# Optimization experiments

Measured on AMD Instinct MI355X. Metric: run time of the kernel, lower is better.

Reference implementation:

```python
import jax, jax.numpy as jnp
import numpy as np

N, B, D = 2048, 2, 512
H, R = 8, 3
C = D // H  # head dim = 64


def setup_inputs() -> dict:
    key = jax.random.key(0)
    ks = jax.random.split(key, 12)
    x_q = jax.random.normal(ks[0], (N, B, D), jnp.float32)
    x_k = jax.random.normal(ks[1], (N, B, D), jnp.float32)
    x_v = jax.random.normal(ks[2], (N, B, D), jnp.float32)
    attn_mask = jax.random.randint(ks[3], (B, R, N, N), 0, 2).astype(bool)
    # pad the last 128 key positions (realistic padding; avoids all -inf rows)
    key_padding_mask = jnp.zeros((B, N), bool).at[:, -128:].set(True)
    s = 1.0 / np.sqrt(D)
    Wq = jax.random.normal(ks[4], (D, D), jnp.float32) * s
    Wk = jax.random.normal(ks[5], (D, D), jnp.float32) * s
    Wv = jax.random.normal(ks[6], (D, D), jnp.float32) * s
    Wo = jax.random.normal(ks[7], (D, D), jnp.float32) * s
    bq = jnp.zeros((D,), jnp.float32)
    bk = jnp.zeros((D,), jnp.float32)
    bv = jnp.zeros((D,), jnp.float32)
    bo = jnp.zeros((D,), jnp.float32)
    # mask_weight: randn, last column set to sqrt(head_dim) as in __init__
    mask_weight = jax.random.normal(ks[8], (H, R + 1), jnp.float32)
    mask_weight = mask_weight.at[:, -1].set(np.sqrt(C))
    return dict(x_q=x_q, x_k=x_k, x_v=x_v, attn_mask=attn_mask,
                key_padding_mask=key_padding_mask, Wq=Wq, bq=bq, Wk=Wk, bk=bk,
                Wv=Wv, bv=bv, Wo=Wo, bo=bo, mask_weight=mask_weight)


def _split_heads(x):
    # (n, b, h*c) -> (b, h, n, c)
    n, b, _ = x.shape
    return jnp.transpose(x.reshape(n, b, H, C), (1, 2, 0, 3))


def reference(x_q, x_k, x_v, attn_mask, key_padding_mask,
              Wq, bq, Wk, bk, Wv, bv, Wo, bo, mask_weight):
    q = _split_heads(x_q @ Wq + bq)  # (b,h,n,c)
    k = _split_heads(x_k @ Wk + bk)
    v = _split_heads(x_v @ Wv + bv)

    # relative bias: softmax over edge-type weights, scaled per head
    rel_w = jax.nn.softmax(mask_weight[:, :-1], axis=-1)  # (h,r)
    inv_mask = (~attn_mask).astype(jnp.float32)           # (b,r,n,m)
    rel = jnp.einsum('hr,h,brnm->bhnm', rel_w, mask_weight[:, -1], inv_mask)
    rel = jnp.where(key_padding_mask[:, None, None, :], -jnp.inf, rel)

    # scaled dot-product attention (torch default scale = 1/sqrt(head_dim))
    scores = jnp.einsum('bhnc,bhmc->bhnm', q, k) * (1.0 / np.sqrt(C))
    attn = jax.nn.softmax(scores + rel, axis=-1)
    o = jnp.einsum('bhnm,bhmc->bhnc', attn, v)

    # (b,h,n,c) -> (n,b,h*c)
    n = o.shape[2]
    o = jnp.transpose(o, (2, 0, 1, 3)).reshape(n, o.shape[0], H * C)
    return o @ Wo + bo
```

## Files before the change

kernel.cpp:

```cpp
#include <hip/hip_runtime.h>
#include <hip/hip_bf16.h>

#define NN 2048
#define LOG2E 1.4426950408889634f

typedef unsigned int u32;
typedef unsigned short u16;
typedef unsigned char u8;

typedef __attribute__((ext_vector_type(8))) short short8;
typedef __attribute__((ext_vector_type(4))) float f32x4;

__device__ __forceinline__ u16 f2bf(float f){
  __hip_bfloat16 h = __float2bfloat16(f);
  return *reinterpret_cast<u16*>(&h);
}
__device__ __forceinline__ float bf1(u16 u){ return __uint_as_float(((u32)u) << 16); }
__device__ __forceinline__ u32 pack2(float a, float b){
  return (u32)f2bf(a) | ((u32)f2bf(b) << 16);
}
__device__ __forceinline__ void gload16(const void* g, void* l){
  __builtin_amdgcn_global_load_lds((const __attribute__((address_space(1))) u32*)g,
                                   (__attribute__((address_space(3))) u32*)l, 16, 0, 0);
}

__global__ __launch_bounds__(256)
void prep_k(const int* __restrict__ am, const int* __restrict__ kp,
            u8* __restrict__ cmb)
{
  const size_t tid  = (size_t)blockIdx.x * 256 + threadIdx.x;
  const size_t base = tid * 4;
  const int row = (int)(base >> 11);
  const int m0  = (int)(base & 2047);
  const int b = row >> 11, n = row & 2047;
  const size_t e0 = (((size_t)(b*3) * NN) + n) * NN + m0;
  const int4 a0 = *reinterpret_cast<const int4*>(am + e0);
  const int4 a1 = *reinterpret_cast<const int4*>(am + e0 + (size_t)NN*NN);
  const int4 a2 = *reinterpret_cast<const int4*>(am + e0 + 2*(size_t)NN*NN);
  const int4 kv = *reinterpret_cast<const int4*>(kp + (size_t)b*NN + m0);
  const int a0v[4] = {a0.x,a0.y,a0.z,a0.w};
  const int a1v[4] = {a1.x,a1.y,a1.z,a1.w};
  const int a2v[4] = {a2.x,a2.y,a2.z,a2.w};
  const int kvv[4] = {kv.x,kv.y,kv.z,kv.w};
  uchar4 out;
  u8* o = (u8*)&out;
  #pragma unroll
  for (int i = 0; i < 4; ++i)
    o[i] = (u8)((a0v[i]?1:0) | (a1v[i]?2:0) | (a2v[i]?4:0) | (kvv[i]?8:0));
  *reinterpret_cast<uchar4*>(cmb + base) = out;
}

__global__ __launch_bounds__(256)
void trw4_k(const float* __restrict__ W0, const float* __restrict__ W1,
            const float* __restrict__ W2, const float* __restrict__ W3,
            u16* __restrict__ WT)
{
  __shared__ float tile[32][33];
  const int zz = blockIdx.z;
  const float* W = (zz == 0) ? W0 : (zz == 1) ? W1 : (zz == 2) ? W2 : W3;
  u16* dst = WT + (size_t)zz * 262144;
  const int t = threadIdx.x;
  const int k0 = blockIdx.x * 32, n0 = blockIdx.y * 32;
  const int c = t & 31, r = t >> 5;
  #pragma unroll
  for (int i = 0; i < 4; ++i)
    tile[r + 8*i][c] = W[(size_t)(k0 + r + 8*i) * 512 + n0 + c];
  __syncthreads();
  #pragma unroll
  for (int i = 0; i < 4; ++i)
    dst[(size_t)(n0 + r + 8*i) * 512 + k0 + c] = f2bf(tile[c][r + 8*i]);
}

__global__ __launch_bounds__(256)
void trw_k(const float* __restrict__ W, u16* __restrict__ WT)
{
  __shared__ float tile[32][33];
  const int t = threadIdx.x;
  const int k0 = blockIdx.x * 32, n0 = blockIdx.y * 32;
  const int c = t & 31, r = t >> 5;
  #pragma unroll
  for (int i = 0; i < 4; ++i)
    tile[r + 8*i][c] = W[(size_t)(k0 + r + 8*i) * 512 + n0 + c];
  __syncthreads();
  #pragma unroll
  for (int i = 0; i < 4; ++i)
    WT[(size_t)(n0 + r + 8*i) * 512 + k0 + c] = f2bf(tile[c][r + 8*i]);
}

template<int BN, bool SCATTER, bool ABF16, bool OUTF32>
__device__ __forceinline__
void gemm_core(const void* __restrict__ Av, const u16* __restrict__ WT,
               const float* __restrict__ bias, void* __restrict__ Cd,
               float scale, int m0, int n0)
{
  constexpr int NI  = BN / 64;
  constexpr int WNL = BN / 32;
  __shared__ u16 As[2][64*64];
  __shared__ u16 Ws[2][BN*64];

  const int t = threadIdx.x;
  const int lane = t & 63;
  const int w = t >> 6;
  const int g = lane >> 4, r15 = lane & 15;
  const int wn = w * (BN/4);

  const int arow = t >> 2, akc = (t & 3) * 16, as0 = (t & 3) * 2;
  const int wrn = (BN==128) ? (t>>1) : (t>>2);
  const int wkc = (BN==128) ? ((t&1)*32) : ((t&3)*16);
  const int wsb = (BN==128) ? ((t&1)*4)  : ((t&3)*2);

  uint4  war[WNL];
  uint4  aab[2];
  float4 aaf[4];

  auto loadA = [&](int k0){
    if constexpr (ABF16) {
      const u16* A = (const u16*)Av;
      aab[0] = *reinterpret_cast<const uint4*>(A + (size_t)(m0+arow)*512 + k0 + akc);
      aab[1] = *reinterpret_cast<const uint4*>(A + (size_t)(m0+arow)*512 + k0 + akc + 8);
    } else {
      const float* A = (const float*)Av;
      #pragma unroll
      for (int q = 0; q < 4; ++q)
        aaf[q] = *reinterpret_cast<const float4*>(A + (size_t)(m0+arow)*512 + k0 + akc + 4*q);
    }
  };
  auto loadW = [&](int k0){
    #pragma unroll
    for (int i = 0; i < WNL; ++i)
      war[i] = *reinterpret_cast<const uint4*>(WT + (size_t)(n0+wrn)*512 + k0 + wkc + 8*i);
  };
  auto writeA = [&](int bf){
    uint4 v0, v1;
    if constexpr (ABF16) { v0 = aab[0]; v1 = aab[1]; }
    else {
      v0.x = pack2(aaf[0].x, aaf[0].y); v0.y = pack2(aaf[0].z, aaf[0].w);
      v0.z = pack2(aaf[1].x, aaf[1].y); v0.w = pack2(aaf[1].z, aaf[1].w);
      v1.x = pack2(aaf[2].x, aaf[2].y); v1.y = pack2(aaf[2].z, aaf[2].w);
      v1.z = pack2(aaf[3].x, aaf[3].y); v1.w = pack2(aaf[3].z, aaf[3].w);
    }
    *reinterpret_cast<uint4*>(&As[bf][arow*64 + (((as0  ) ^ (arow&7)) << 3)]) = v0;
    *reinterpret_cast<uint4*>(&As[bf][arow*64 + (((as0+1) ^ (arow&7)) << 3)]) = v1;
  };
  auto writeW = [&](int bf){
    #pragma unroll
    for (int i = 0; i < WNL; ++i)
      *reinterpret_cast<uint4*>(&Ws[bf][wrn*64 + (((wsb+i) ^ (wrn&7)) << 3)]) = war[i];
  };

  const f32x4 fz = {0.f,0.f,0.f,0.f};
  f32x4 acc[4][NI];
  #pragma unroll
  for (int mi = 0; mi < 4; ++mi)
    #pragma unroll
    for (int ni = 0; ni < NI; ++ni) acc[mi][ni] = fz;

  loadA(0); loadW(0);
  writeA(0); writeW(0);
  __syncthreads();

  for (int kt = 0; kt < 8; ++kt) {
    const int cur = kt & 1;
    if (kt < 7) { loadA((kt+1)*64); loadW((kt+1)*64); }
    #pragma unroll
    for (int ks = 0; ks < 2; ++ks) {
      short8 bfr[NI], afr[4];
      #pragma unroll
      for (int ni = 0; ni < NI; ++ni) {
        const int n = wn + 16*ni + r15;
        bfr[ni] = *reinterpret_cast<const short8*>(&Ws[cur][n*64 + (((ks*4+g) ^ (n&7)) << 3)]);
      }
      #pragma unroll
      for (int mi = 0; mi < 4; ++mi) {
        const int m = 16*mi + r15;
        afr[mi] = *reinterpret_cast<const short8*>(&As[cur][m*64 + (((ks*4+g) ^ (m&7)) << 3)]);
      }
      #pragma unroll
      for (int mi = 0; mi < 4; ++mi)
        #pragma unroll
        for (int ni = 0; ni < NI; ++ni)
          acc[mi][ni] = __builtin_amdgcn_mfma_f32_16x16x32_bf16(afr[mi], bfr[ni], acc[mi][ni], 0, 0, 0);
    }
    if (kt < 7) { writeA(cur^1); writeW(cur^1); }
    __syncthreads();
  }

  float bia[NI];
  #pragma unroll
  for (int ni = 0; ni < NI; ++ni) bia[ni] = bias[n0 + wn + 16*ni + r15];
  #pragma unroll
  for (int mi = 0; mi < 4; ++mi) {
    #pragma unroll
    for (int ni = 0; ni < NI; ++ni) {
      #pragma unroll
      for (int j = 0; j < 4; ++j) {
        const int row = m0 + 16*mi + 4*g + j;
        const int col = n0 + wn + 16*ni + r15;
        const float v = (acc[mi][ni][j] + bia[ni]) * scale;
        if constexpr (SCATTER) {
          const int bb = row & 1, ntok = row >> 1;
          const int h = col >> 6, c = col & 63;
          ((u16*)Cd)[(((size_t)(bb*8 + h) * NN + ntok) * 64) + c] = f2bf(v);
        } else if constexpr (OUTF32) {
          ((float*)Cd)[(size_t)row * 512 + col] = v;
        } else {
          ((u16*)Cd)[(size_t)row * 512 + col] = f2bf(v);
        }
      }
    }
  }
}

__global__ __launch_bounds__(256)
void gemm_qkv(const float* __restrict__ x0, const float* __restrict__ x1,
              const float* __restrict__ x2, const u16* __restrict__ WT3,
              const float* __restrict__ b0, const float* __restrict__ b1,
              const float* __restrict__ b2, u16* __restrict__ dst, float qscale)
{
  const int z = blockIdx.z;
  const float* A    = (z == 0) ? x0 : (z == 1) ? x1 : x2;
  const float* bias = (z == 0) ? b0 : (z == 1) ? b1 : b2;
  gemm_core<128, true, false, false>(A, WT3 + (size_t)z*262144, bias,
                                     dst + (size_t)z*2097152,
                                     (z == 0) ? qscale : 1.0f,
                                     blockIdx.x*64, blockIdx.y*128);
}

__global__ __launch_bounds__(256)
void gemm_wo(const u16* __restrict__ Ob, const u16* __restrict__ WT,
             const float* __restrict__ bias, float* __restrict__ out)
{
  gemm_core<64, false, true, true>(Ob, WT, bias, out, 1.0f,
                                   blockIdx.x*64, blockIdx.y*64);
}

__global__ __launch_bounds__(512)
void attn_mfma(const u16* __restrict__ Q, const u16* __restrict__ K,
               const u16* __restrict__ V, const u8* __restrict__ cmb,
               const float* __restrict__ mw, u16* __restrict__ O,
               u16* __restrict__ Opart, float2* __restrict__ Ml, int kspan)
{
  __shared__ u16 Ks[2][64*64];
  __shared__ u16 Vs[2][64*64];
  __shared__ u16 Ps[8][16*64];
  __shared__ float lut[16];

  const int t = threadIdx.x;
  const int lane = t & 63;
  const int w = t >> 6;
  const int g = lane >> 4;
  const int r15 = lane & 15;
  const int bh = blockIdx.y;
  const int z = blockIdx.z;
  const int b = bh >> 3, h = bh & 7;
  const int n0 = blockIdx.x * 128;
  const int nq = n0 + w*16 + r15;
  const int k_beg = z * kspan;
  const float NEGINF = -__builtin_inff();

  if (t < 16) {
    const float mw0 = mw[h*4+0], mw1 = mw[h*4+1], mw2 = mw[h*4+2];
    const float msc = mw[h*4+3];
    const float mxw = fmaxf(mw0, fmaxf(mw1, mw2));
    const float e0 = __expf(mw0-mxw), e1 = __expf(mw1-mxw), e2 = __expf(mw2-mxw);
    const float inv = msc / (e0+e1+e2);
    float v = ((t & 1) ? 0.f : e0*inv) + ((t & 2) ? 0.f : e1*inv)
            + ((t & 4) ? 0.f : e2*inv);
    lut[t] = (t & 8) ? NEGINF : v * LOG2E;
  }

  const u16* qrow = Q + ((size_t)bh*NN + nq)*64;
  const short8 bq0 = *reinterpret_cast<const short8*>(qrow + 8*g);
  const short8 bq1 = *reinterpret_cast<const short8*>(qrow + 32 + 8*g);

  const u8* crow = cmb + ((size_t)(b*NN + nq))*NN;
  const u16* Kbase = K + (size_t)bh*NN*64;
  const u16* Vbase = V + (size_t)bh*NN*64;

  float m_run = NEGINF, l_run = 0.f;
  const f32x4 fz = {0.f, 0.f, 0.f, 0.f};
  f32x4 oacc[4] = {fz, fz, fz, fz};

  const int sm  = t >> 3;
  const int ssl = t & 7;
  const int kcol = (ssl ^ (sm & 7)) * 8;
  const int sc0 = (t & 7) * 8;

  uint4 vreg;
  auto gloadK = [&](int m0, int bf){
    gload16(Kbase + (size_t)(m0 + sm)*64 + kcol, &Ks[bf][w*512 + (lane << 3)]);
  };
  auto loadV = [&](int m0){
    vreg = *reinterpret_cast<const uint4*>(Vbase + (size_t)(m0 + sm)*64 + sc0);
  };
  auto writeV = [&](int bf){
    u16 e[8];
    e[0]=vreg.x&0xffff; e[1]=vreg.x>>16; e[2]=vreg.y&0xffff; e[3]=vreg.y>>16;
    e[4]=vreg.z&0xffff; e[5]=vreg.z>>16; e[6]=vreg.w&0xffff; e[7]=vreg.w>>16;
    #pragma unroll
    for (int i = 0; i < 8; ++i) {
      const int c = sc0 + i;
      Vs[bf][c*64 + ((((sm>>3) ^ (c&7) ^ (c>>3)) << 3) | (sm & 7))] = e[i];
    }
  };

  const int ntiles = kspan >> 6;
  gloadK(k_beg, 0);
  loadV(k_beg);
  writeV(0);
  __syncthreads();

  for (int it = 0; it < ntiles; ++it) {
    const int cur = it & 1;
    const int m0 = k_beg + it * 64;
    const bool more = (it + 1 < ntiles);
    if (more) { gloadK(m0 + 64, cur ^ 1); loadV(m0 + 64); }

    float sv[4][4];
    __builtin_amdgcn_s_setprio(1);
    #pragma unroll
    for (int kt = 0; kt < 4; ++kt) {
      const int key = 16*kt + r15;
      const short8 a0 = *reinterpret_cast<const short8*>(&Ks[cur][key*64 + (((g  ) ^ (key&7)) << 3)]);
      const short8 a1 = *reinterpret_cast<const short8*>(&Ks[cur][key*64 + (((g+4) ^ (key&7)) << 3)]);
      f32x4 s = fz;
      s = __builtin_amdgcn_mfma_f32_16x16x32_bf16(a0, bq0, s, 0, 0, 0);
      s = __builtin_amdgcn_mfma_f32_16x16x32_bf16(a1, bq1, s, 0, 0, 0);
      const u32 cw = *reinterpret_cast<const u32*>(crow + m0 + 16*kt + 4*g);
      #pragma unroll
      for (int j = 0; j < 4; ++j)
        sv[kt][j] = s[j] + lut[(cw >> (8*j)) & 0xfu];
    }
    __builtin_amdgcn_s_setprio(0);
    float pmax = NEGINF;
    #pragma unroll
    for (int kt = 0; kt < 4; ++kt)
      #pragma unroll
      for (int j = 0; j < 4; ++j) pmax = fmaxf(pmax, sv[kt][j]);
    float tmax = pmax;
    tmax = fmaxf(tmax, __shfl_xor(tmax, 16));
    tmax = fmaxf(tmax, __shfl_xor(tmax, 32));

    const bool skip = __all((m_run != NEGINF) && (tmax <= m_run + 10.0f));
    float nm = m_run, sc = 1.0f;
    if (!skip) {
      nm = fmaxf(m_run, tmax);
      if (nm != NEGINF) { sc = exp2f(m_run - nm); m_run = nm; }
      #pragma unroll
      for (int ct = 0; ct < 4; ++ct) oacc[ct] *= sc;
    }

    float psum = 0.f;
    #pragma unroll
    for (int kt = 0; kt < 4; ++kt) {
      float p[4];
      #pragma unroll
      for (int j = 0; j < 4; ++j) {
        p[j] = (nm == NEGINF) ? 0.f : exp2f(sv[kt][j] - nm);
        psum += p[j];
      }
      const int slot = 2*kt + (g >> 1);
      const int off  = 4 * (g & 1);
      *reinterpret_cast<ushort4*>(&Ps[w][r15*64 + ((slot ^ (r15 & 7)) << 3) + off]) =
        make_ushort4(f2bf(p[0]), f2bf(p[1]), f2bf(p[2]), f2bf(p[3]));
    }
    psum += __shfl_xor(psum, 16);
    psum += __shfl_xor(psum, 32);
    l_run = l_run * sc + psum;

    const short8 bp0 = *reinterpret_cast<const short8*>(&Ps[w][r15*64 + (((g  ) ^ (r15 & 7)) << 3)]);
    const short8 bp1 = *reinterpret_cast<const short8*>(&Ps[w][r15*64 + (((g+4) ^ (r15 & 7)) << 3)]);
    __builtin_amdgcn_s_setprio(1);
    #pragma unroll
    for (int ct = 0; ct < 4; ++ct) {
      const int c = 16*ct + r15;
      const short8 av0 = *reinterpret_cast<const short8*>(
        &Vs[cur][c*64 + ((((g  ) ^ (c&7) ^ (c>>3))) << 3)]);
      const short8 av1 = *reinterpret_cast<const short8*>(
        &Vs[cur][c*64 + ((((g+4) ^ (c&7) ^ (c>>3))) << 3)]);
      oacc[ct] = __builtin_amdgcn_mfma_f32_16x16x32_bf16(av0, bp0, oacc[ct], 0, 0, 0);
      oacc[ct] = __builtin_amdgcn_mfma_f32_16x16x32_bf16(av1, bp1, oacc[ct], 0, 0, 0);
    }
    __builtin_amdgcn_s_setprio(0);

    if (more) writeV(cur ^ 1);
    __syncthreads();
  }

  if (Opart) {
    u16* orow = Opart + (((size_t)(z*16 + bh)) * NN + nq) * 64;
    #pragma unroll
    for (int ct = 0; ct < 4; ++ct)
      *reinterpret_cast<ushort4*>(orow + 16*ct + 4*g) =
        make_ushort4(f2bf(oacc[ct][0]), f2bf(oacc[ct][1]),
                     f2bf(oacc[ct][2]), f2bf(oacc[ct][3]));
    if (g == 0)
      Ml[((size_t)(z*16 + bh)) * NN + nq] = make_float2(m_run, l_run);
  } else {
    const float rinv = 1.f / l_run;
    #pragma unroll
    for (int ct = 0; ct < 4; ++ct) {
      u16* dst = O + ((size_t)(nq*2 + b))*512 + h*64 + 16*ct + 4*g;
      *reinterpret_cast<ushort4*>(dst) =
        make_ushort4(f2bf(oacc[ct][0]*rinv), f2bf(oacc[ct][1]*rinv),
                     f2bf(oacc[ct][2]*rinv), f2bf(oacc[ct][3]*rinv));
    }
  }
}

__global__ __launch_bounds__(256)
void combine_k(const u16* __restrict__ Opart, const float2* __restrict__ Ml,
               u16* __restrict__ Ob, int nsplit)
{
  const int t = threadIdx.x;
  const int lane = t & 63, w = t >> 6;
  const int q = blockIdx.x * 4 + w;
  const int bh = blockIdx.y;
  const int b = bh >> 3, h = bh & 7;

  float M = -__builtin_inff();
  for (int s = 0; s < nsplit; ++s)
    M = fmaxf(M, Ml[((size_t)(s*16 + bh)) * NN + q].x);

  float num = 0.f, den = 0.f;
  for (int s = 0; s < nsplit; ++s) {
    const float2 ml = Ml[((size_t)(s*16 + bh)) * NN + q];
    const float ws = (ml.x == -__builtin_inff()) ? 0.f : exp2f(ml.x - M);
    den += ws * ml.y;
    num += ws * bf1(Opart[(((size_t)(s*16 + bh)) * NN + q) * 64 + lane]);
  }
  const float r = (den > 0.f) ? num / den : 0.f;
  Ob[((size_t)(q*2 + b)) * 512 + h*64 + lane] = f2bf(r);
}

extern "C" void kernel_launch(void* const* d_in, const int* in_sizes, int n_in,
                              void* d_out, int out_size, void* d_ws, size_t ws_size,
                              hipStream_t stream)
{
  const float* xq = (const float*)d_in[0];
  const float* xk = (const float*)d_in[1];
  const float* xv = (const float*)d_in[2];
  const int*   am = (const int*)d_in[3];
  const int*   kp = (const int*)d_in[4];
  const float* Wq = (const float*)d_in[5];
  const float* bq = (const float*)d_in[6];
  const float* Wk = (const float*)d_in[7];
  const float* bk = (const float*)d_in[8];
  const float* Wv = (const float*)d_in[9];
  const float* bv = (const float*)d_in[10];
  const float* Wo = (const float*)d_in[11];
  const float* bo = (const float*)d_in[12];
  const float* mw = (const float*)d_in[13];

  u16* Qb = (u16*)d_ws;
  u16* Kb = Qb + (size_t)16*NN*64;
  u16* Vb = Kb + (size_t)16*NN*64;
  u16* Ob = Vb + (size_t)16*NN*64;
  u8*  cmb = (u8*)(Ob + (size_t)4096*512);
  u8*  R   = cmb + (size_t)2*NN*NN;

  u16* Opart = (u16*)R;
  const size_t base_bytes = (size_t)(R - (u8*)d_ws);
  int nsplit = 1;
  for (int s = 4; s >= 1; s >>= 1) {
    const size_t need = base_bytes + (size_t)s * 16 * NN * (64*2 + 8);
    if (need <= ws_size) { nsplit = s; break; }
  }
  float2* Ml = (float2*)(Opart + (size_t)nsplit * 16 * NN * 64);
  const bool split = (base_bytes + (size_t)16*NN*(64*2+8) <= ws_size);

  u16* WT4 = (u16*)(R + (size_t)18*1024*1024);
  const bool wt4_ok = (base_bytes + (size_t)18*1024*1024 + 4*262144*2 <= ws_size);
  u16* WT3 = wt4_ok ? WT4 : (u16*)R;
  u16* WTo = wt4_ok ? (WT4 + 3*262144) : Qb;

  prep_k<<<(2*NN*NN/4 + 255)/256, 256, 0, stream>>>(am, kp, cmb);

  const float qscale = 0.125f * LOG2E;
  if (wt4_ok) {
    trw4_k<<<dim3(16, 16, 4), 256, 0, stream>>>(Wq, Wk, Wv, Wo, WT4);
  } else {
    trw4_k<<<dim3(16, 16, 3), 256, 0, stream>>>(Wq, Wk, Wv, Wo, WT3);
  }
  gemm_qkv<<<dim3(64, 4, 3), 256, 0, stream>>>(xq, xk, xv, WT3, bq, bk, bv, Qb, qscale);

  if (split) {
    attn_mfma<<<dim3(16, 16, nsplit), 512, 0, stream>>>(Qb, Kb, Vb, cmb, mw, Ob,
                                                        Opart, Ml, NN / nsplit);
    combine_k<<<dim3(NN/4, 16), 256, 0, stream>>>(Opart, Ml, Ob, nsplit);
  } else {
    attn_mfma<<<dim3(16, 16, 1), 512, 0, stream>>>(Qb, Kb, Vb, cmb, mw, Ob,
                                                   nullptr, nullptr, NN);
  }
  if (!wt4_ok)
    trw_k<<<dim3(16, 16), 256, 0, stream>>>(Wo, WTo);
  gemm_wo<<<dim3(64, 8), 256, 0, stream>>>(Ob, WTo, bo, (float*)d_out);
}
```

Baseline: 121.4 us.

## Pre-transpose V and fuse mask prep into QKV GEMM launch

Adds a kernel that transposes V per head into a column-major layout so the attention kernel can stream V tiles with direct global-to-LDS loads instead of a register load followed by a scattered per-element LDS write. It also merges the mask-combining kernel and the QKV projection GEMM into one launch, with block ranges picking the role, so the two independent jobs can overlap. This adds an extra transpose pass over V and more workspace use. The non-split fallback passes VT rather than VTp, which may be wrong when the workspace is small.

```diff
diff --git a/kernel.cpp b/kernel.cpp
--- a/kernel.cpp
+++ b/kernel.cpp
@@ -22,32 +22,6 @@
 __device__ __forceinline__ void gload16(const void* g, void* l){
   __builtin_amdgcn_global_load_lds((const __attribute__((address_space(1))) u32*)g,
                                    (__attribute__((address_space(3))) u32*)l, 16, 0, 0);
-}
-
-__global__ __launch_bounds__(256)
-void prep_k(const int* __restrict__ am, const int* __restrict__ kp,
-            u8* __restrict__ cmb)
-{
-  const size_t tid  = (size_t)blockIdx.x * 256 + threadIdx.x;
-  const size_t base = tid * 4;
-  const int row = (int)(base >> 11);
-  const int m0  = (int)(base & 2047);
-  const int b = row >> 11, n = row & 2047;
-  const size_t e0 = (((size_t)(b*3) * NN) + n) * NN + m0;
-  const int4 a0 = *reinterpret_cast<const int4*>(am + e0);
-  const int4 a1 = *reinterpret_cast<const int4*>(am + e0 + (size_t)NN*NN);
-  const int4 a2 = *reinterpret_cast<const int4*>(am + e0 + 2*(size_t)NN*NN);
-  const int4 kv = *reinterpret_cast<const int4*>(kp + (size_t)b*NN + m0);
-  const int a0v[4] = {a0.x,a0.y,a0.z,a0.w};
-  const int a1v[4] = {a1.x,a1.y,a1.z,a1.w};
-  const int a2v[4] = {a2.x,a2.y,a2.z,a2.w};
-  const int kvv[4] = {kv.x,kv.y,kv.z,kv.w};
-  uchar4 out;
-  u8* o = (u8*)&out;
-  #pragma unroll
-  for (int i = 0; i < 4; ++i)
-    o[i] = (u8)((a0v[i]?1:0) | (a1v[i]?2:0) | (a2v[i]?4:0) | (kvv[i]?8:0));
-  *reinterpret_cast<uchar4*>(cmb + base) = out;
 }
 
 __global__ __launch_bounds__(256)
@@ -85,6 +59,38 @@
   #pragma unroll
   for (int i = 0; i < 4; ++i)
     WT[(size_t)(n0 + r + 8*i) * 512 + k0 + c] = f2bf(tile[c][r + 8*i]);
+}
+
+__global__ __launch_bounds__(256)
+void trv_k(const u16* __restrict__ Vb, u16* __restrict__ VT)
+{
+  __shared__ u16 tile[64][72];
+  const int bh = blockIdx.y;
+  const int n0 = blockIdx.x * 64;
+  const int t = threadIdx.x;
+  {
+    const int r = t >> 2, cs = (t & 3) * 16;
+    const u16* src = Vb + ((size_t)bh*NN + n0 + r)*64 + cs;
+    const uint4 v0 = *reinterpret_cast<const uint4*>(src);
+    const uint4 v1 = *reinterpret_cast<const uint4*>(src + 8);
+    const u32 wds[8] = {v0.x,v0.y,v0.z,v0.w,v1.x,v1.y,v1.z,v1.w};
+    #pragma unroll
+    for (int i = 0; i < 8; ++i) {
+      tile[r][cs + 2*i]     = (u16)(wds[i] & 0xffff);
+      tile[r][cs + 2*i + 1] = (u16)(wds[i] >> 16);
+    }
+  }
+  __syncthreads();
+  {
+    const int c = t >> 2, ns = (t & 3) * 16;
+    u32 owds[8];
+    #pragma unroll
+    for (int i = 0; i < 8; ++i)
+      owds[i] = (u32)tile[ns + 2*i][c] | ((u32)tile[ns + 2*i + 1][c] << 16);
+    u16* dst = VT + ((size_t)bh*64 + c)*NN + n0 + ns;
+    *reinterpret_cast<uint4*>(dst)     = make_uint4(owds[0],owds[1],owds[2],owds[3]);
+    *reinterpret_cast<uint4*>(dst + 8) = make_uint4(owds[4],owds[5],owds[6],owds[7]);
+  }
 }
 
 template<int BN, bool SCATTER, bool ABF16, bool OUTF32>
@@ -212,18 +218,46 @@
 }
 
 __global__ __launch_bounds__(256)
-void gemm_qkv(const float* __restrict__ x0, const float* __restrict__ x1,
-              const float* __restrict__ x2, const u16* __restrict__ WT3,
-              const float* __restrict__ b0, const float* __restrict__ b1,
-              const float* __restrict__ b2, u16* __restrict__ dst, float qscale)
-{
-  const int z = blockIdx.z;
-  const float* A    = (z == 0) ? x0 : (z == 1) ? x1 : x2;
-  const float* bias = (z == 0) ? b0 : (z == 1) ? b1 : b2;
-  gemm_core<128, true, false, false>(A, WT3 + (size_t)z*262144, bias,
-                                     dst + (size_t)z*2097152,
-                                     (z == 0) ? qscale : 1.0f,
-                                     blockIdx.x*64, blockIdx.y*128);
+void front_k(const float* __restrict__ x0, const float* __restrict__ x1,
+             const float* __restrict__ x2, const u16* __restrict__ WT3,
+             const float* __restrict__ b0, const float* __restrict__ b1,
+             const float* __restrict__ b2, u16* __restrict__ dst, float qscale,
+             const int* __restrict__ am, const int* __restrict__ kp,
+             u8* __restrict__ cmb)
+{
+  const int bid = blockIdx.x;
+  if (bid < 768) {
+    const int z  = bid >> 8;
+    const int rem = bid & 255;
+    const int bx = rem & 63, by = rem >> 6;
+    const float* A    = (z == 0) ? x0 : (z == 1) ? x1 : x2;
+    const float* bias = (z == 0) ? b0 : (z == 1) ? b1 : b2;
+    gemm_core<128, true, false, false>(A, WT3 + (size_t)z*262144, bias,
+                                       dst + (size_t)z*2097152,
+                                       (z == 0) ? qscale : 1.0f,
+                                       bx*64, by*128);
+  } else {
+    const size_t tid  = (size_t)(bid - 768) * 256 + threadIdx.x;
+    const size_t base = tid * 4;
+    const int row = (int)(base >> 11);
+    const int m0  = (int)(base & 2047);
+    const int b = row >> 11, n = row & 2047;
+    const size_t e0 = (((size_t)(b*3) * NN) + n) * NN + m0;
+    const int4 a0 = *reinterpret_cast<const int4*>(am + e0);
+    const int4 a1 = *reinterpret_cast<const int4*>(am + e0 + (size_t)NN*NN);
+    const int4 a2 = *reinterpret_cast<const int4*>(am + e0 + 2*(size_t)NN*NN);
+    const int4 kv = *reinterpret_cast<const int4*>(kp + (size_t)b*NN + m0);
+    const int a0v[4] = {a0.x,a0.y,a0.z,a0.w};
+    const int a1v[4] = {a1.x,a1.y,a1.z,a1.w};
+    const int a2v[4] = {a2.x,a2.y,a2.z,a2.w};
+    const int kvv[4] = {kv.x,kv.y,kv.z,kv.w};
+    uchar4 out;
+    u8* o = (u8*)&out;
+    #pragma unroll
+    for (int i = 0; i < 4; ++i)
+      o[i] = (u8)((a0v[i]?1:0) | (a1v[i]?2:0) | (a2v[i]?4:0) | (kvv[i]?8:0));
+    *reinterpret_cast<uchar4*>(cmb + base) = out;
+  }
 }
 
 __global__ __launch_bounds__(256)
@@ -236,7 +270,7 @@
 
 __global__ __launch_bounds__(512)
 void attn_mfma(const u16* __restrict__ Q, const u16* __restrict__ K,
-               const u16* __restrict__ V, const u8* __restrict__ cmb,
+               const u16* __restrict__ VT, const u8* __restrict__ cmb,
                const float* __restrict__ mw, u16* __restrict__ O,
                u16* __restrict__ Opart, float2* __restrict__ Ml, int kspan)
 {
@@ -274,8 +308,8 @@
   const short8 bq1 = *reinterpret_cast<const short8*>(qrow + 32 + 8*g);
 
   const u8* crow = cmb + ((size_t)(b*NN + nq))*NN;
-  const u16* Kbase = K + (size_t)bh*NN*64;
-  const u16* Vbase = V + (size_t)bh*NN*64;
+  const u16* Kbase  = K  + (size_t)bh*NN*64;
+  const u16* VTbase = VT + (size_t)bh*64*NN;
 
   float m_run = NEGINF, l_run = 0.f;
   const f32x4 fz = {0.f, 0.f, 0.f, 0.f};
@@ -284,37 +318,26 @@
   const int sm  = t >> 3;
   const int ssl = t & 7;
   const int kcol = (ssl ^ (sm & 7)) * 8;
-  const int sc0 = (t & 7) * 8;
-
-  uint4 vreg;
+  const int vc   = t >> 3;
+  const int vcol = ((t & 7) ^ (vc & 7) ^ (vc >> 3)) * 8;
+
   auto gloadK = [&](int m0, int bf){
-    gload16(Kbase + (size_t)(m0 + sm)*64 + kcol, &Ks[bf][w*512 + (lane << 3)]);
+    gload16(Kbase + (size_t)(m0 + sm)*64 + kcol, &Ks[bf][t << 3]);
   };
-  auto loadV = [&](int m0){
-    vreg = *reinterpret_cast<const uint4*>(Vbase + (size_t)(m0 + sm)*64 + sc0);
-  };
-  auto writeV = [&](int bf){
-    u16 e[8];
-    e[0]=vreg.x&0xffff; e[1]=vreg.x>>16; e[2]=vreg.y&0xffff; e[3]=vreg.y>>16;
-    e[4]=vreg.z&0xffff; e[5]=vreg.z>>16; e[6]=vreg.w&0xffff; e[7]=vreg.w>>16;
-    #pragma unroll
-    for (int i = 0; i < 8; ++i) {
-      const int c = sc0 + i;
-      Vs[bf][c*64 + ((((sm>>3) ^ (c&7) ^ (c>>3)) << 3) | (sm & 7))] = e[i];
-    }
+  auto gloadV = [&](int m0, int bf){
+    gload16(VTbase + (size_t)vc*NN + m0 + vcol, &Vs[bf][t << 3]);
   };
 
   const int ntiles = kspan >> 6;
   gloadK(k_beg, 0);
-  loadV(k_beg);
-  writeV(0);
+  gloadV(k_beg, 0);
   __syncthreads();
 
   for (int it = 0; it < ntiles; ++it) {
     const int cur = it & 1;
     const int m0 = k_beg + it * 64;
     const bool more = (it + 1 < ntiles);
-    if (more) { gloadK(m0 + 64, cur ^ 1); loadV(m0 + 64); }
+    if (more) { gloadK(m0 + 64, cur ^ 1); gloadV(m0 + 64, cur ^ 1); }
 
     float sv[4][4];
     __builtin_amdgcn_s_setprio(1);
@@ -383,7 +406,6 @@
     }
     __builtin_amdgcn_s_setprio(0);
 
-    if (more) writeV(cur ^ 1);
     __syncthreads();
   }
 
@@ -473,23 +495,23 @@
   const bool wt4_ok = (base_bytes + (size_t)18*1024*1024 + 4*262144*2 <= ws_size);
   u16* WT3 = wt4_ok ? WT4 : (u16*)R;
   u16* WTo = wt4_ok ? (WT4 + 3*262144) : Qb;
-
-  prep_k<<<(2*NN*NN/4 + 255)/256, 256, 0, stream>>>(am, kp, cmb);
+  u16* VT  = (u16*)(R + (size_t)20*1024*1024);
+  const bool vt_ok = (base_bytes + (size_t)20*1024*1024 + (size_t)16*64*NN*2 <= ws_size);
+  u16* VTp = vt_ok ? VT : Ob;
 
   const float qscale = 0.125f * LOG2E;
-  if (wt4_ok) {
-    trw4_k<<<dim3(16, 16, 4), 256, 0, stream>>>(Wq, Wk, Wv, Wo, WT4);
-  } else {
-    trw4_k<<<dim3(16, 16, 3), 256, 0, stream>>>(Wq, Wk, Wv, Wo, WT3);
-  }
-  gemm_qkv<<<dim3(64, 4, 3), 256, 0, stream>>>(xq, xk, xv, WT3, bq, bk, bv, Qb, qscale);
+  trw4_k<<<dim3(16, 16, wt4_ok ? 4 : 3), 256, 0, stream>>>(Wq, Wk, Wv, Wo,
+                                                           wt4_ok ? WT4 : WT3);
+  front_k<<<dim3(768 + 8192), 256, 0, stream>>>(xq, xk, xv, WT3, bq, bk, bv, Qb,
+                                                qscale, am, kp, cmb);
+  trv_k<<<dim3(32, 16), 256, 0, stream>>>(Vb, VTp);
 
   if (split) {
-    attn_mfma<<<dim3(16, 16, nsplit), 512, 0, stream>>>(Qb, Kb, Vb, cmb, mw, Ob,
+    attn_mfma<<<dim3(16, 16, nsplit), 512, 0, stream>>>(Qb, Kb, VTp, cmb, mw, Ob,
                                                         Opart, Ml, NN / nsplit);
     combine_k<<<dim3(NN/4, 16), 256, 0, stream>>>(Opart, Ml, Ob, nsplit);
   } else {
-    attn_mfma<<<dim3(16, 16, 1), 512, 0, stream>>>(Qb, Kb, Vb, cmb, mw, Ob,
+    attn_mfma<<<dim3(16, 16, 1), 512, 0, stream>>>(Qb, Kb, VT, cmb, mw, Ob,
                                                    nullptr, nullptr, NN);
   }
   if (!wt4_ok)
```

New measurement: 123.5 us. Within noise of the previous version (+1.7%).
